# Performance work log

Measured on AMD Instinct MI355X. Metric: run time of the kernel, lower is better.

The kernel has to match this reference:

```python
import jax, jax.numpy as jnp
import numpy as np

C, H, W = 128, 376, 1248
N = 200000

def setup_inputs() -> dict:
    key = jax.random.key(0)
    k1, k2, k3 = jax.random.split(key, 3)
    feature_map = jax.random.normal(k1, (C, H, W), dtype=jnp.float32)
    # u in [0, W-2), v in [0, H-2) so that floor+1 stays in-bounds
    u = jax.random.uniform(k2, (N,), dtype=jnp.float32) * (W - 2)
    v = jax.random.uniform(k3, (N,), dtype=jnp.float32) * (H - 2)
    target_uv = jnp.stack([u, v], axis=1)  # [N, 2]
    return {"feature_map": feature_map, "target_uv": target_uv, "downscale": 1}

def reference(feature_map, target_uv, downscale):
    # feature_map: [C, H, W], target_uv: [N, 2] (u, v)
    u = target_uv[:, 0] / downscale
    v = target_uv[:, 1] / downscale
    u_lo = u.astype(jnp.int32)
    v_lo = v.astype(jnp.int32)
    u_hi = u_lo + 1
    v_hi = v_lo + 1
    du = u - u_lo.astype(jnp.float32)
    dv = v - v_lo.astype(jnp.float32)
    # Four gathers [C, N] + bilinear blend
    out = (feature_map[:, v_lo, u_lo] * ((1 - dv) * (1 - du))
           + feature_map[:, v_hi, u_lo] * (dv * (1 - du))
           + feature_map[:, v_lo, u_hi] * ((1 - dv) * du)
           + feature_map[:, v_hi, u_hi] * (dv * du))
    return out  # [C, N]
```

## Files before the change

kernel.cpp:

```cpp
#include <hip/hip_runtime.h>
#include <hip/hip_fp16.h>

constexpr int C = 128, H = 376, W = 1248;
constexpr int HW = H * W;

constexpr int BIN  = 14;
constexpr int BU   = (W + BIN - 1) / BIN;
constexpr int BV   = (H + BIN - 1) / BIN;
constexpr int NBINS = BU * BV;
constexpr int CAP  = 160;
constexpr int CPG  = 16;
constexpr int NCG  = C / CPG;
constexpr int ROWS = BIN + 1;
constexpr int CHROW = 4;
constexpr int RWF  = CHROW * 4;
constexpr int CH_CHUNKS = ROWS * CHROW + 1;
constexpr int CH_F = CH_CHUNKS * 4;
constexpr int BLK_CHUNKS = CPG * CH_CHUNKS;
constexpr int K4T  = 192;
constexpr int STG = (BLK_CHUNKS + K4T - 1) / K4T;

typedef float vfloat4 __attribute__((ext_vector_type(4)));

__global__ __launch_bounds__(512) void k0_init(int* cursor) {
    for (int i = threadIdx.x + blockIdx.x * 512; i < NBINS; i += gridDim.x * 512)
        cursor[i] = i * CAP;
}

__global__ __launch_bounds__(256) void k3_scatter(const float* __restrict__ uv,
                                                  const int* __restrict__ dsp,
                                                  int* __restrict__ cursor,
                                                  uint2* __restrict__ sorted,
                                                  int* __restrict__ inv, int N) {
    int n = blockIdx.x * 256 + threadIdx.x;
    if (n >= N) return;
    float dsf = (float)dsp[0];
    float2 p = ((const float2*)uv)[n];
    float u = p.x / dsf, v = p.y / dsf;
    int ul = (int)u, vl = (int)v;
    float du = u - (float)ul, dv = v - (float)vl;
    int bin = (vl / BIN) * BU + (ul / BIN);
    int pos = atomicAdd(cursor + bin, 1);
    uint2 rec;
    rec.x = (unsigned)(ul | (vl << 16));
    rec.y = (unsigned)(du * 65535.f + 0.5f) | ((unsigned)(dv * 65535.f + 0.5f) << 16);
    sorted[pos] = rec;
    inv[n] = pos;
}

__global__ __launch_bounds__(K4T) void k4_resample(const float* __restrict__ fmap,
                                                   const uint2* __restrict__ sorted,
                                                   const int* __restrict__ cursor,
                                                   __half* __restrict__ mid, int N) {
    __shared__ float lds[BLK_CHUNKS * 4];

    int bin = blockIdx.x >> 3;
    int cg  = blockIdx.x & 7;
    int bu  = bin % BU;
    int bv  = bin / BU;
    int u0  = bu * BIN;
    int v0  = bv * BIN;
    int cb  = cg * CPG;
    int tid = threadIdx.x;
    int s   = bin * CAP;
    int e   = cursor[bin];

    vfloat4 stg[STG];
#pragma unroll
    for (int i = 0; i < STG; ++i) {
        int k = tid + i * K4T;
        if (k < BLK_CHUNKS) {
            int ch   = k / CH_CHUNKS;
            int rem  = k - ch * CH_CHUNKS;
            int rem2 = min(rem, ROWS * CHROW - 1);
            int r    = rem2 / CHROW;
            int c4   = rem2 - r * CHROW;
            int gr   = min(v0 + r, H - 1);
            int gc   = min(u0 + c4 * 4, W - 4);
            stg[i] = *(const vfloat4*)(fmap + (size_t)(cb + ch) * HW + (size_t)gr * W + gc);
        }
    }
    __builtin_amdgcn_sched_barrier(0);
#pragma unroll
    for (int i = 0; i < STG; ++i) {
        int k = tid + i * K4T;
        if (k < BLK_CHUNKS)
            *(vfloat4*)&lds[k * 4] = stg[i];
    }
    __syncthreads();

    int q = tid & 3;
    const float* chbase = &lds[q * 4 * CH_F];
    __half* midbase = mid + ((size_t)cg * (size_t)NBINS * CAP) * 16 + q * 4;
    for (int p = s + (tid >> 2); p < e; p += (K4T / 4)) {
        uint2 pt = sorted[p];
        int ul = (int)(pt.x & 0xffffu);
        int vl = (int)(pt.x >> 16);
        float du = (float)(pt.y & 0xffffu) * (1.0f / 65535.0f);
        float dv = (float)(pt.y >> 16)     * (1.0f / 65535.0f);

        float w00 = (1.0f - dv) * (1.0f - du);
        float w10 = dv * (1.0f - du);
        float w01 = (1.0f - dv) * du;
        float w11 = dv * du;

        const float* base = chbase + (vl - v0) * RWF + (ul - u0);
        float r[4];
#pragma unroll
        for (int c = 0; c < 4; ++c) {
            float f00 = base[c * CH_F];
            float f01 = base[c * CH_F + 1];
            float f10 = base[c * CH_F + RWF];
            float f11 = base[c * CH_F + RWF + 1];
            r[c] = f00 * w00 + f10 * w10 + f01 * w01 + f11 * w11;
        }
        union { __half2 h2[2]; uint2 u; } pk;
        pk.h2[0] = __floats2half2_rn(r[0], r[1]);
        pk.h2[1] = __floats2half2_rn(r[2], r[3]);
        *(uint2*)(midbase + (size_t)p * 16) = pk.u;
    }
}

__global__ __launch_bounds__(256) void k5_permute(const __half* __restrict__ mid,
                                                  const int* __restrict__ inv,
                                                  float* __restrict__ out, int N) {
    __shared__ float tile[64 * 132];
    __shared__ int   sp[64];
    int n0 = blockIdx.x * 64;
    int t  = threadIdx.x;
    int cnt = min(64, N - n0);

    if (t < 64) sp[t] = (t < cnt) ? inv[n0 + t] : 0;
    __syncthreads();

    int j  = t >> 2;
    int q4 = t & 3;
    constexpr size_t CGSTRIDE = (size_t)NBINS * CAP;
    uint2 g[8];
#pragma unroll
    for (int r = 0; r < 8; ++r) {
        if (j < cnt)
            g[r] = *(const uint2*)(mid + ((size_t)r * CGSTRIDE + sp[j]) * 16 + q4 * 4);
    }
#pragma unroll
    for (int r = 0; r < 8; ++r) {
        if (j < cnt) {
            union { uint2 u; __half2 h2[2]; } pk; pk.u = g[r];
            float2 f0 = __half22float2(pk.h2[0]);
            float2 f1 = __half22float2(pk.h2[1]);
            vfloat4 w = {f0.x, f0.y, f1.x, f1.y};
            *(vfloat4*)&tile[j * 132 + r * 16 + q4 * 4] = w;
        }
    }
    __syncthreads();

    int jj = t & 63;
    for (int s = 0; s < 32; ++s) {
        int c = s * 4 + (t >> 6);
        if (jj < cnt)
            __builtin_nontemporal_store(tile[jj * 132 + c], out + (size_t)c * N + n0 + jj);
    }
}

constexpr int F_CPG = 2;
constexpr int F_CG  = C / F_CPG;
constexpr int F_GPX = F_CG / 8;

__global__ __launch_bounds__(256) void fallback_kernel(
    const float* __restrict__ fmap, const float* __restrict__ uv,
    const int* __restrict__ dsp, float* __restrict__ out, int N, int NBX)
{
    int bid = blockIdx.x;
    int xcd = bid & 7;
    int jj  = bid >> 3;
    int g_local = jj / NBX;
    int nb      = jj - g_local * NBX;
    int g   = xcd * F_GPX + g_local;

    int n = nb * 256 + threadIdx.x;
    if (n >= N) return;

    float dsf = (float)dsp[0];
    float2 p = ((const float2*)uv)[n];
    float u = p.x / dsf, v = p.y / dsf;
    int u_lo = (int)u, v_lo = (int)v;
    float du = u - (float)u_lo, dv = v - (float)v_lo;

    float w00 = (1.0f - dv) * (1.0f - du);
    float w10 = dv * (1.0f - du);
    float w01 = (1.0f - dv) * du;
    float w11 = dv * du;

    int cbase = g * F_CPG;
    const float* fp = fmap + (size_t)cbase * HW + (size_t)v_lo * W + u_lo;
    float*       op = out  + (size_t)cbase * N + n;
#pragma unroll
    for (int c = 0; c < F_CPG; ++c) {
        float f00 = fp[0], f01 = fp[1], f10 = fp[W], f11 = fp[W + 1];
        float r = f00 * w00 + f10 * w10 + f01 * w01 + f11 * w11;
        __builtin_nontemporal_store(r, op);
        fp += HW; op += N;
    }
}

extern "C" void kernel_launch(void* const* d_in, const int* in_sizes, int n_in,
                              void* d_out, int out_size, void* d_ws, size_t ws_size,
                              hipStream_t stream)
{
    const float* fmap = (const float*)d_in[0];
    const float* uv   = (const float*)d_in[1];
    const int*   dsp  = (const int*)d_in[2];
    float*       out  = (float*)d_out;

    int N = in_sizes[1] / 2;

    size_t off_cursor = 0;
    size_t off_inv    = 16384;
    size_t off_sorted = off_inv + (((size_t)N * 4 + 255) & ~(size_t)255);
    size_t off_mid    = off_sorted + (((size_t)NBINS * CAP * 8 + 255) & ~(size_t)255);
    size_t need       = off_mid + (size_t)NBINS * CAP * 32 * NCG;

    if (ws_size < need) {
        int NBX = (N + 255) / 256;
        dim3 grid(NBX * F_CG);
        fallback_kernel<<<grid, dim3(256), 0, stream>>>(fmap, uv, dsp, out, N, NBX);
        return;
    }

    char* ws = (char*)d_ws;
    int*    cursor = (int*)(ws + off_cursor);
    int*    inv    = (int*)(ws + off_inv);
    uint2*  sorted = (uint2*)(ws + off_sorted);
    __half* mid    = (__half*)(ws + off_mid);

    int nb = (N + 255) / 256;
    k0_init<<<4, 512, 0, stream>>>(cursor);
    k3_scatter<<<nb, 256, 0, stream>>>(uv, dsp, cursor, sorted, inv, N);
    k4_resample<<<NBINS * NCG, K4T, 0, stream>>>(fmap, sorted, cursor, mid, N);
    k5_permute<<<(N + 63) / 64, 256, 0, stream>>>(mid, inv, out, N);
}
```

Before: 184.0 us.

## Process two bins per resample block and prefetch the second tile during compute

Each k4_resample block now handles a pair of adjacent bins for one channel group instead of a single bin, and the block size grows from 192 to 256 threads. The global loads for the second bin's feature tile are issued into registers right after the first tile is written to LDS, so they overlap with the first bin's bilinear compute. This is meant to hide global load latency and halve the number of block launches. In exchange it adds an extra barrier per bin and keeps the staging registers live across the compute loop, which may reduce occupancy.

```diff
diff --git a/kernel.cpp b/kernel.cpp
--- a/kernel.cpp
+++ b/kernel.cpp
@@ -17,8 +17,7 @@
 constexpr int CH_CHUNKS = ROWS * CHROW + 1;
 constexpr int CH_F = CH_CHUNKS * 4;
 constexpr int BLK_CHUNKS = CPG * CH_CHUNKS;
-constexpr int K4T  = 192;
-constexpr int STG = (BLK_CHUNKS + K4T - 1) / K4T;
+constexpr int STG = (BLK_CHUNKS + 255) / 256;
 
 typedef float vfloat4 __attribute__((ext_vector_type(4)));
 
@@ -48,76 +47,109 @@
     inv[n] = pos;
 }
 
-__global__ __launch_bounds__(K4T) void k4_resample(const float* __restrict__ fmap,
+__global__ __launch_bounds__(256) void k4_resample(const float* __restrict__ fmap,
                                                    const uint2* __restrict__ sorted,
                                                    const int* __restrict__ cursor,
                                                    __half* __restrict__ mid, int N) {
     __shared__ float lds[BLK_CHUNKS * 4];
 
-    int bin = blockIdx.x >> 3;
-    int cg  = blockIdx.x & 7;
-    int bu  = bin % BU;
-    int bv  = bin / BU;
-    int u0  = bu * BIN;
-    int v0  = bv * BIN;
+    int pairI = blockIdx.x >> 3;
+    int cg    = blockIdx.x & 7;
+    int bin0  = pairI * 2;
     int cb  = cg * CPG;
     int tid = threadIdx.x;
-    int s   = bin * CAP;
-    int e   = cursor[bin];
+    int q   = tid & 3;
+    const float* chbase = &lds[q * 4 * CH_F];
+    __half* midcg = mid + ((size_t)cg * (size_t)NBINS * CAP) * 16 + q * 4;
+
+    int e0 = cursor[bin0];
+    int e1 = cursor[bin0 + 1];
+
+    int chv[STG], rv_[STG], c4v[STG];
+    bool ok[STG];
+#pragma unroll
+    for (int i = 0; i < STG; ++i) {
+        int k = tid + i * 256;
+        ok[i] = (k < BLK_CHUNKS);
+        int kk = ok[i] ? k : 0;
+        int ch   = kk / CH_CHUNKS;
+        int rem  = kk - ch * CH_CHUNKS;
+        int rem2 = min(rem, ROWS * CHROW - 1);
+        chv[i] = ch;
+        rv_[i] = rem2 / CHROW;
+        c4v[i] = (rem2 - rv_[i] * CHROW) * 4;
+    }
 
     vfloat4 stg[STG];
-#pragma unroll
-    for (int i = 0; i < STG; ++i) {
-        int k = tid + i * K4T;
-        if (k < BLK_CHUNKS) {
-            int ch   = k / CH_CHUNKS;
-            int rem  = k - ch * CH_CHUNKS;
-            int rem2 = min(rem, ROWS * CHROW - 1);
-            int r    = rem2 / CHROW;
-            int c4   = rem2 - r * CHROW;
-            int gr   = min(v0 + r, H - 1);
-            int gc   = min(u0 + c4 * 4, W - 4);
-            stg[i] = *(const vfloat4*)(fmap + (size_t)(cb + ch) * HW + (size_t)gr * W + gc);
-        }
-    }
-    __builtin_amdgcn_sched_barrier(0);
-#pragma unroll
-    for (int i = 0; i < STG; ++i) {
-        int k = tid + i * K4T;
-        if (k < BLK_CHUNKS)
-            *(vfloat4*)&lds[k * 4] = stg[i];
-    }
-    __syncthreads();
-
-    int q = tid & 3;
-    const float* chbase = &lds[q * 4 * CH_F];
-    __half* midbase = mid + ((size_t)cg * (size_t)NBINS * CAP) * 16 + q * 4;
-    for (int p = s + (tid >> 2); p < e; p += (K4T / 4)) {
-        uint2 pt = sorted[p];
-        int ul = (int)(pt.x & 0xffffu);
-        int vl = (int)(pt.x >> 16);
-        float du = (float)(pt.y & 0xffffu) * (1.0f / 65535.0f);
-        float dv = (float)(pt.y >> 16)     * (1.0f / 65535.0f);
-
-        float w00 = (1.0f - dv) * (1.0f - du);
-        float w10 = dv * (1.0f - du);
-        float w01 = (1.0f - dv) * du;
-        float w11 = dv * du;
-
-        const float* base = chbase + (vl - v0) * RWF + (ul - u0);
-        float r[4];
-#pragma unroll
-        for (int c = 0; c < 4; ++c) {
-            float f00 = base[c * CH_F];
-            float f01 = base[c * CH_F + 1];
-            float f10 = base[c * CH_F + RWF];
-            float f11 = base[c * CH_F + RWF + 1];
-            r[c] = f00 * w00 + f10 * w10 + f01 * w01 + f11 * w11;
-        }
-        union { __half2 h2[2]; uint2 u; } pk;
-        pk.h2[0] = __floats2half2_rn(r[0], r[1]);
-        pk.h2[1] = __floats2half2_rn(r[2], r[3]);
-        *(uint2*)(midbase + (size_t)p * 16) = pk.u;
+    {
+        int bu = bin0 % BU, bv = bin0 / BU;
+        int u0 = bu * BIN, v0 = bv * BIN;
+#pragma unroll
+        for (int i = 0; i < STG; ++i) {
+            if (ok[i]) {
+                int gr = min(v0 + rv_[i], H - 1);
+                int gc = min(u0 + c4v[i], W - 4);
+                stg[i] = *(const vfloat4*)(fmap + (size_t)(cb + chv[i]) * HW + (size_t)gr * W + gc);
+            }
+        }
+    }
+
+#pragma unroll
+    for (int b = 0; b < 2; ++b) {
+        int bin = bin0 + b;
+        int bu = bin % BU, bv = bin / BU;
+        int u0 = bu * BIN, v0 = bv * BIN;
+        int s = bin * CAP;
+        int e = b ? e1 : e0;
+
+#pragma unroll
+        for (int i = 0; i < STG; ++i)
+            if (ok[i]) *(vfloat4*)&lds[(tid + i * 256) * 4] = stg[i];
+        __syncthreads();
+
+        if (b == 0) {
+            int bin1 = bin0 + 1;
+            int bu1 = bin1 % BU, bv1 = bin1 / BU;
+            int u01 = bu1 * BIN, v01 = bv1 * BIN;
+#pragma unroll
+            for (int i = 0; i < STG; ++i) {
+                if (ok[i]) {
+                    int gr = min(v01 + rv_[i], H - 1);
+                    int gc = min(u01 + c4v[i], W - 4);
+                    stg[i] = *(const vfloat4*)(fmap + (size_t)(cb + chv[i]) * HW + (size_t)gr * W + gc);
+                }
+            }
+            __builtin_amdgcn_sched_barrier(0);
+        }
+
+        for (int p = s + (tid >> 2); p < e; p += 64) {
+            uint2 pt = sorted[p];
+            int ul = (int)(pt.x & 0xffffu);
+            int vl = (int)(pt.x >> 16);
+            float du = (float)(pt.y & 0xffffu) * (1.0f / 65535.0f);
+            float dv = (float)(pt.y >> 16)     * (1.0f / 65535.0f);
+
+            float w00 = (1.0f - dv) * (1.0f - du);
+            float w10 = dv * (1.0f - du);
+            float w01 = (1.0f - dv) * du;
+            float w11 = dv * du;
+
+            const float* base = chbase + (vl - v0) * RWF + (ul - u0);
+            float r[4];
+#pragma unroll
+            for (int c = 0; c < 4; ++c) {
+                float f00 = base[c * CH_F];
+                float f01 = base[c * CH_F + 1];
+                float f10 = base[c * CH_F + RWF];
+                float f11 = base[c * CH_F + RWF + 1];
+                r[c] = f00 * w00 + f10 * w10 + f01 * w01 + f11 * w11;
+            }
+            union { __half2 h2[2]; uint2 u; } pk;
+            pk.h2[0] = __floats2half2_rn(r[0], r[1]);
+            pk.h2[1] = __floats2half2_rn(r[2], r[3]);
+            *(uint2*)(midcg + (size_t)p * 16) = pk.u;
+        }
+        __syncthreads();
     }
 }
 
@@ -236,6 +268,6 @@
     int nb = (N + 255) / 256;
     k0_init<<<4, 512, 0, stream>>>(cursor);
     k3_scatter<<<nb, 256, 0, stream>>>(uv, dsp, cursor, sorted, inv, N);
-    k4_resample<<<NBINS * NCG, K4T, 0, stream>>>(fmap, sorted, cursor, mid, N);
+    k4_resample<<<(NBINS / 2) * NCG, 256, 0, stream>>>(fmap, sorted, cursor, mid, N);
     k5_permute<<<(N + 63) / 64, 256, 0, stream>>>(mid, inv, out, N);
 }
```

Result: faster. 165.3 us (-10.2%).
